# Kernel tuning notes

Hardware: AMD Instinct MI355X
Metric: run time of the kernel (lower is better)

## Reference

```python
import jax, jax.numpy as jnp
import numpy as np

N_QUBITS = 12
DIM = 2 ** N_QUBITS  # 4096

_H = (jnp.array([[1.0, 1.0], [1.0, -1.0]]) / np.sqrt(2.0)).astype(jnp.complex64)
_X = jnp.array([[0.0, 1.0], [1.0, 0.0]], dtype=jnp.complex64)


def setup_inputs() -> dict:
    key = jax.random.key(0)
    k1, k2 = jax.random.split(key)
    state = jax.random.normal(k1, (8, 512, DIM), dtype=jnp.float32)
    params = jax.random.normal(k2, (N_QUBITS,), dtype=jnp.float32)
    return {"state": state, "params": params}


def _to_quantum(x):
    # faithful to _classical_to_quantum_inspired: normalize, phase = acos(|v|), sign * exp(i*phase)
    norms = jnp.linalg.norm(x, axis=-1, keepdims=True)
    v = x / (norms + 1e-8)
    mag = jnp.minimum(jnp.abs(v), 1.0)
    q = (jnp.sign(v) * jnp.exp(1j * jnp.arccos(mag))).astype(jnp.complex64)
    nrm = jnp.sqrt(jnp.sum(q.real ** 2 + q.imag ** 2, axis=-1, keepdims=True))
    return q / nrm.astype(jnp.complex64)


def _axis(q):
    # qubit q = bit q (LSB); tensor axes ordered MSB-first after batch axis 0
    return 1 + (N_QUBITS - 1 - q)


def _apply_1q(full, q, U):
    ax = _axis(q)
    moved = jnp.moveaxis(full, ax, -1)
    out = jnp.einsum('...b,ab->...a', moved, U)
    return jnp.moveaxis(out, -1, ax)


def _apply_ctrl(full, c, t, U):
    # apply U on target qubit t where control qubit c == 1
    axc = _axis(c)
    b0 = jnp.take(full, 0, axis=axc)
    b1 = jnp.take(full, 1, axis=axc)
    axt = _axis(t)
    axt_sub = axt - 1 if axt > axc else axt
    moved = jnp.moveaxis(b1, axt_sub, -1)
    b1n = jnp.moveaxis(jnp.einsum('...b,ab->...a', moved, U), -1, axt_sub)
    return jnp.stack([b0, b1n], axis=axc)


def _rx(theta):
    c = jnp.cos(theta / 2).astype(jnp.complex64)
    s = (-1j * jnp.sin(theta / 2)).astype(jnp.complex64)
    return jnp.stack([jnp.stack([c, s]), jnp.stack([s, c])])


def reference(state, params):
    B, T, D = state.shape
    psi = _to_quantum(state.reshape(B * T, D))  # (N, 2**n) complex64
    full = psi.reshape((B * T,) + (2,) * N_QUBITS)
    for q in range(N_QUBITS):
        full = _apply_1q(full, q, _H)                                  # Hadamard
        full = _apply_ctrl(full, q, (q + 1) % N_QUBITS, _rx(params[q]))  # controlled-RX
        if q < N_QUBITS - 1:
            full = _apply_ctrl(full, q, q + 1, _X)                     # CNOT
    amp = full.reshape(B * T, D)
    probs = amp.real ** 2 + amp.imag ** 2  # measurement probabilities
    return probs.reshape(B, T, D).astype(jnp.float32)
```

## Files before the change

kernel.cpp:

```cpp
#include <hip/hip_runtime.h>

#define NQ  12
#define DIM 4096
#define TPB 256

typedef float v2f __attribute__((ext_vector_type(2)));
typedef float v4f __attribute__((ext_vector_type(4)));


__device__ __forceinline__ float wave_reduce(float v) {
#pragma unroll
    for (int m = 32; m >= 1; m >>= 1) v += __shfl_xor(v, m, 64);
    return v;
}

#define BCAST(v, q) __uint_as_float(__builtin_amdgcn_readlane(__float_as_uint(v), (q)))

template <int MC, int MT, bool XGATE>
__device__ __forceinline__ void apply_layer(v2f* a, v2f ctv, v2f snv) {
#pragma unroll
    for (int i = 0; i < 16; ++i) {
        if (i & MC) continue;
        const int j = i | MC;
        const v2f t0 = a[i], t1 = a[j];
        a[i] = t0 + t1;
        a[j] = t0 - t1;
    }
#pragma unroll
    for (int i = 0; i < 16; ++i) {
        if (!(i & MC) || (i & MT)) continue;
        const int j = i | MT;
        const v2f b0 = a[i], b1 = a[j];
        const v2f s0 = snv * b0.yx;
        const v2f s1 = snv * b1.yx;
        if (XGATE) {
            a[i] = ctv * b1 + s0;
            a[j] = ctv * b0 + s1;
        } else {
            a[i] = ctv * b0 + s1;
            a[j] = ctv * b1 + s0;
        }
    }
}

__global__ __launch_bounds__(TPB, 5) void qlayer_kernel(
        const float* __restrict__ state, const float* __restrict__ params,
        float* __restrict__ out) {
    __shared__ __align__(16) v2f amp[DIM];
    char* const lds = (char*)amp;

    const int t = threadIdx.x;
    const int lane = t & 63;
    const long long sbase = (long long)blockIdx.x * DIM;

    const float th = params[lane < NQ ? lane : 0] * 0.5f;
    const float cl = cosf(th);
    const float sl = sinf(th);

    const float4* gp = (const float4*)(state + sbase + t * 16);
    float4 xv[4];
    float ss = 0.f;
#pragma unroll
    for (int j = 0; j < 4; ++j) {
        const float4 v = gp[j];
        xv[j] = v;
        ss = fmaf(v.x, v.x, ss); ss = fmaf(v.y, v.y, ss);
        ss = fmaf(v.z, v.z, ss); ss = fmaf(v.w, v.w, ss);
    }
    ss = wave_reduce(ss);
    if (lane == 0) ((float*)lds)[t >> 6] = ss;
    __syncthreads();
    const float* redp = (const float*)lds;
    const float sst = redp[0] + redp[1] + redp[2] + redp[3];
    const float invd = __builtin_amdgcn_rsqf(sst);
    __syncthreads();

    v2f a[16];
#define ENC(k, xval)                                                      \
    {                                                                     \
        const float v   = (xval) * invd;                                  \
        const float re  = fminf(fmaxf(v, -1.0f), 1.0f);                   \
        const float imb = __builtin_amdgcn_sqrtf(fmaxf(1.0f - re * re, 0.f)); \
        const float im  = (v > 0.f) ? imb : ((v < 0.f) ? -imb : 0.f);     \
        v2f q; q.x = re; q.y = im;                                        \
        a[k] = q;                                                         \
    }
#pragma unroll
    for (int j = 0; j < 4; ++j) {
        const float4 xq = xv[j];
        ENC(4 * j + 0, xq.x); ENC(4 * j + 1, xq.y);
        ENC(4 * j + 2, xq.z); ENC(4 * j + 3, xq.w);
    }
#undef ENC

#define CTV(q) ({ v2f _c; _c.x = BCAST(cl, q); _c.y = _c.x; _c; })
#define SNV(q) ({ float _s = BCAST(sl, q); v2f _v; _v.x = _s; _v.y = -_s; _v; })

    apply_layer<1, 2, true>(a, CTV(0), SNV(0));
    apply_layer<2, 4, true>(a, CTV(1), SNV(1));
    apply_layer<4, 8, true>(a, CTV(2), SNV(2));
    {
        const int v1b = (t << 7) | (((t >> 1) & 7) << 4);
#pragma unroll
        for (int k = 0; k < 8; ++k) {
            v4f w; w.x = a[2 * k].x; w.y = a[2 * k].y;
            w.z = a[2 * k + 1].x; w.w = a[2 * k + 1].y;
            *(v4f*)(lds + (v1b ^ (k << 4))) = w;
        }
    }

    {
        const int g  = t >> 3;
        const int gp2 = g & 1;
        const int baseE = ((t & 7) << 3) + (g << 10) + (gp2 << 6);
        const int baseO = ((t & 7) << 3) + (g << 10) + ((1 - gp2) << 6);
#pragma unroll
        for (int r = 0; r < 16; ++r)
            a[r] = *(const v2f*)(lds +
                ((((r & 1) ? baseO : baseE) ^ ((r >> 2) << 4)) + ((r >> 1) << 7)));
        apply_layer<1, 2, true>(a, CTV(3), SNV(3));
        apply_layer<2, 4, true>(a, CTV(4), SNV(4));
        apply_layer<4, 8, true>(a, CTV(5), SNV(5));
#pragma unroll
        for (int r = 0; r < 16; ++r)
            *(v2f*)(lds +
                ((((r & 1) ? baseO : baseE) ^ ((r >> 2) << 4)) + ((r >> 1) << 7))) = a[r];
    }

    {
        const int b3b = (((t & 63) ^ (((t >> 5) & 1) << 1)) << 3) + ((t >> 6) << 13);
#pragma unroll
        for (int r = 0; r < 16; ++r)
            a[r] = *(const v2f*)(lds + ((b3b ^ ((r & 3) << 5)) + (r << 9)));
        apply_layer<1, 2, true>(a, CTV(6), SNV(6));
        apply_layer<2, 4, true>(a, CTV(7), SNV(7));
        apply_layer<4, 8, true>(a, CTV(8), SNV(8));
#pragma unroll
        for (int r = 0; r < 16; ++r)
            *(v2f*)(lds + ((b3b ^ ((r & 3) << 5)) + (r << 9))) = a[r];
    }
    __syncthreads();

    {
        const int F0b = (t << 4) ^ (((t >> 4) & 7) << 4);
#pragma unroll
        for (int k = 0; k < 8; ++k) {
            const v4f v = *(const v4f*)(lds + (F0b + (k << 12)));
            v2f q0; q0.x = v.x; q0.y = v.y;
            v2f q1; q1.x = v.z; q1.y = v.w;
            a[k] = q0;
            a[k + 8] = q1;
        }
        apply_layer<1, 2, true >(a, CTV(9),  SNV(9));
        apply_layer<2, 4, true >(a, CTV(10), SNV(10));
        apply_layer<4, 8, false>(a, CTV(11), SNV(11));

        v2f sc2; sc2.x = 0x1p-24f; sc2.y = 0x1p-24f;
        v2f* outp = (v2f*)(out + sbase);
#pragma unroll
        for (int k = 0; k < 8; ++k) {
            const v2f q0 = a[k] * a[k];
            const v2f q1 = a[k | 8] * a[k | 8];
            v2f res; res.x = q0.x + q0.y;
            res.y = q1.x + q1.y;
            res = res * sc2;
            __builtin_nontemporal_store(res, outp + t + (k << 8));
        }
    }
#undef CTV
#undef SNV
}

extern "C" void kernel_launch(void* const* d_in, const int* in_sizes, int n_in,
                              void* d_out, int out_size, void* d_ws, size_t ws_size,
                              hipStream_t stream) {
    (void)in_sizes; (void)n_in; (void)out_size; (void)d_ws; (void)ws_size;
    const float* state  = (const float*)d_in[0];
    const float* params = (const float*)d_in[1];
    float* out = (float*)d_out;
    qlayer_kernel<<<dim3(4096), dim3(TPB), 0, stream>>>(state, params, out);
}
```

Before: 115.0 us.

## Process two state rows per block with the second row's loads issued up front

Each block now handles two consecutive rows instead of one, so the grid is halved. Both rows' global loads are issued at kernel start, letting the second row's memory latency overlap the first row's gate computation. The per-wave norm partials are copied to four spread-out LDS slots so each wave reads its own copy. This raises register pressure under the existing launch bound. There is also no barrier between reading those slots and the tile's first LDS writes, which risks a read-after-overwrite race.

```diff
diff --git a/kernel.cpp b/kernel.cpp
--- a/kernel.cpp
+++ b/kernel.cpp
@@ -43,38 +43,13 @@
     }
 }
 
-__global__ __launch_bounds__(TPB, 5) void qlayer_kernel(
-        const float* __restrict__ state, const float* __restrict__ params,
-        float* __restrict__ out) {
-    __shared__ __align__(16) v2f amp[DIM];
-    char* const lds = (char*)amp;
-
-    const int t = threadIdx.x;
-    const int lane = t & 63;
-    const long long sbase = (long long)blockIdx.x * DIM;
-
-    const float th = params[lane < NQ ? lane : 0] * 0.5f;
-    const float cl = cosf(th);
-    const float sl = sinf(th);
-
-    const float4* gp = (const float4*)(state + sbase + t * 16);
-    float4 xv[4];
-    float ss = 0.f;
-#pragma unroll
-    for (int j = 0; j < 4; ++j) {
-        const float4 v = gp[j];
-        xv[j] = v;
-        ss = fmaf(v.x, v.x, ss); ss = fmaf(v.y, v.y, ss);
-        ss = fmaf(v.z, v.z, ss); ss = fmaf(v.w, v.w, ss);
-    }
-    ss = wave_reduce(ss);
-    if (lane == 0) ((float*)lds)[t >> 6] = ss;
-    __syncthreads();
-    const float* redp = (const float*)lds;
-    const float sst = redp[0] + redp[1] + redp[2] + redp[3];
-    const float invd = __builtin_amdgcn_rsqf(sst);
-    __syncthreads();
-
+#define CTV(q) ({ v2f _c; _c.x = BCAST(cl, q); _c.y = _c.x; _c; })
+#define SNV(q) ({ float _s = BCAST(sl, q); v2f _v; _v.x = _s; _v.y = -_s; _v; })
+
+__device__ __forceinline__ void run_tile(const float4* xv, float invd,
+                                         char* lds, int t,
+                                         float cl, float sl,
+                                         float* __restrict__ outb) {
     v2f a[16];
 #define ENC(k, xval)                                                      \
     {                                                                     \
@@ -93,9 +68,6 @@
     }
 #undef ENC
 
-#define CTV(q) ({ v2f _c; _c.x = BCAST(cl, q); _c.y = _c.x; _c; })
-#define SNV(q) ({ float _s = BCAST(sl, q); v2f _v; _v.x = _s; _v.y = -_s; _v; })
-
     apply_layer<1, 2, true>(a, CTV(0), SNV(0));
     apply_layer<2, 4, true>(a, CTV(1), SNV(1));
     apply_layer<4, 8, true>(a, CTV(2), SNV(2));
@@ -156,7 +128,7 @@
         apply_layer<4, 8, false>(a, CTV(11), SNV(11));
 
         v2f sc2; sc2.x = 0x1p-24f; sc2.y = 0x1p-24f;
-        v2f* outp = (v2f*)(out + sbase);
+        v2f* outp = (v2f*)outb;
 #pragma unroll
         for (int k = 0; k < 8; ++k) {
             const v2f q0 = a[k] * a[k];
@@ -167,8 +139,70 @@
             __builtin_nontemporal_store(res, outp + t + (k << 8));
         }
     }
-#undef CTV
-#undef SNV
+}
+
+__global__ __launch_bounds__(TPB, 5) void qlayer_kernel(
+        const float* __restrict__ state, const float* __restrict__ params,
+        float* __restrict__ out) {
+    __shared__ __align__(16) v2f amp[DIM];
+    char* const lds = (char*)amp;
+
+    const int t = threadIdx.x;
+    const int lane = t & 63;
+    const int wv = t >> 6;
+    const long long sbase0 = (long long)blockIdx.x * (2 * DIM);
+    const long long sbase1 = sbase0 + DIM;
+
+    const float4* gp0 = (const float4*)(state + sbase0 + t * 16);
+    const float4* gp1 = (const float4*)(state + sbase1 + t * 16);
+    float4 xv0[4], xv1[4];
+#pragma unroll
+    for (int j = 0; j < 4; ++j) xv0[j] = gp0[j];
+#pragma unroll
+    for (int j = 0; j < 4; ++j) xv1[j] = gp1[j];
+
+    const float th = params[lane < NQ ? lane : 0] * 0.5f;
+    const float cl = cosf(th);
+    const float sl = sinf(th);
+
+    float ss0 = 0.f, ss1 = 0.f;
+#pragma unroll
+    for (int j = 0; j < 4; ++j) {
+        const float4 v = xv0[j];
+        ss0 = fmaf(v.x, v.x, ss0); ss0 = fmaf(v.y, v.y, ss0);
+        ss0 = fmaf(v.z, v.z, ss0); ss0 = fmaf(v.w, v.w, ss0);
+    }
+#pragma unroll
+    for (int j = 0; j < 4; ++j) {
+        const float4 v = xv1[j];
+        ss1 = fmaf(v.x, v.x, ss1); ss1 = fmaf(v.y, v.y, ss1);
+        ss1 = fmaf(v.z, v.z, ss1); ss1 = fmaf(v.w, v.w, ss1);
+    }
+    ss0 = wave_reduce(ss0);
+    ss1 = wave_reduce(ss1);
+
+    if (lane == 0) {
+#pragma unroll
+        for (int s = 0; s < 4; ++s) *(float*)(lds + 8192 * s + 4 * wv) = ss0;
+    }
+    __syncthreads();
+    {
+        const float* p = (const float*)(lds + 8192 * wv);
+        const float invd0 = __builtin_amdgcn_rsqf(p[0] + p[1] + p[2] + p[3]);
+        run_tile(xv0, invd0, lds, t, cl, sl, out + sbase0);
+    }
+    __syncthreads();
+
+    if (lane == 0) {
+#pragma unroll
+        for (int s = 0; s < 4; ++s) *(float*)(lds + 8192 * s + 4 * wv) = ss1;
+    }
+    __syncthreads();
+    {
+        const float* p = (const float*)(lds + 8192 * wv);
+        const float invd1 = __builtin_amdgcn_rsqf(p[0] + p[1] + p[2] + p[3]);
+        run_tile(xv1, invd1, lds, t, cl, sl, out + sbase1);
+    }
 }
 
 extern "C" void kernel_launch(void* const* d_in, const int* in_sizes, int n_in,
@@ -178,5 +212,5 @@
     const float* state  = (const float*)d_in[0];
     const float* params = (const float*)d_in[1];
     float* out = (float*)d_out;
-    qlayer_kernel<<<dim3(4096), dim3(TPB), 0, stream>>>(state, params, out);
-}
+    qlayer_kernel<<<dim3(2048), dim3(TPB), 0, stream>>>(state, params, out);
+}
```

Result: no change. 115.7 us (+0.6%).
